# Kernel optimization log

Measured on AMD Instinct MI355X. Metric: run time of the kernel, lower is better.

The kernel has to match this reference:

```python
import jax, jax.numpy as jnp
import numpy as np
from jax import lax

DN = ('NCHW', 'OIHW', 'NCHW')
NUM_HEADS = 6


def _conv1x1(x, w):
    return lax.conv_general_dilated(x, w, (1, 1), 'VALID', dimension_numbers=DN)


def _dwconv3x3(x, w):
    # depthwise 3x3, groups == channels, padding 1
    return lax.conv_general_dilated(x, w, (1, 1), ((1, 1), (1, 1)),
                                    dimension_numbers=DN,
                                    feature_group_count=w.shape[0])


def setup_inputs() -> dict:
    key = jax.random.key(0)
    ks = jax.random.split(key, 7)
    b, dim, h, w = 4, 192, 128, 128
    inp = {
        'x': jax.random.normal(ks[0], (b, dim, h, w), jnp.float32),
        'ref': jax.random.normal(ks[1], (b, dim, h, w), jnp.float32),
        'w_qkv': jax.random.normal(ks[2], (dim * 3, dim, 1, 1), jnp.float32) * 0.05,
        'w_dw': jax.random.normal(ks[3], (dim * 3, 1, 3, 3), jnp.float32) * 0.1,
        'w_proj': jax.random.normal(ks[4], (dim, dim, 1, 1), jnp.float32) * 0.05,
        'temperature': jnp.ones((NUM_HEADS, 1, 1), jnp.float32),
        'attn_w': 0.2 * jnp.ones((4,), jnp.float32),
    }
    return inp


def reference(x, ref, w_qkv, w_dw, w_proj, temperature, attn_w):
    b, c, h, w = x.shape
    heads = NUM_HEADS
    C = c // heads  # per-head channel dim
    hw = h * w

    qkv = _dwconv3x3(_conv1x1(x, w_qkv), w_dw)        # [b, 3c, h, w]
    ref_qkv = _dwconv3x3(_conv1x1(ref, w_qkv), w_dw)  # shared weights

    q_shared = qkv[:, :c]            # q from x
    k_shared = ref_qkv[:, c:2 * c]   # k from ref
    v_shared = ref_qkv[:, 2 * c:]    # v from ref

    def to_heads(t):  # [b, c, h, w] -> [b, head, C, hw]
        return t.reshape(b, heads, C, hw)

    q = to_heads(q_shared)
    k = to_heads(k_shared)
    v = to_heads(v_shared)

    # L2-normalize along token dim (last axis)
    q = q / jnp.maximum(jnp.linalg.norm(q, axis=-1, keepdims=True), 1e-12)
    k = k / jnp.maximum(jnp.linalg.norm(k, axis=-1, keepdims=True), 1e-12)

    # channel-wise attention: [b, head, C, C]
    attn = jnp.einsum('bhcn,bhdn->bhcd', q, k) * temperature

    ks_list = [int(C / 2), int(C * 2 / 3), int(C * 3 / 4), int(C * 4 / 5)]
    neg_inf = jnp.asarray(-jnp.inf, attn.dtype)

    out = 0.0
    for i, ki in enumerate(ks_list):
        vals = lax.top_k(attn, ki)[0]            # [b, head, C, ki]
        thr = vals[..., -1:]                     # k-th largest per row
        a = jnp.where(attn >= thr, attn, neg_inf)
        a = jax.nn.softmax(a, axis=-1)
        out = out + attn_w[i] * jnp.einsum('bhcd,bhdn->bhcn', a, v)

    out = out.reshape(b, c, h, w)
    return _conv1x1(out, w_proj)
```

## Files before the change

### kernel.cpp

```cpp
#include <hip/hip_runtime.h>
#include <cstdint>
#include <cstddef>

typedef unsigned short u16;
typedef unsigned int u32;
typedef __attribute__((ext_vector_type(2))) float f32x2;
typedef __attribute__((ext_vector_type(4))) float f32x4;
typedef __attribute__((ext_vector_type(8))) short short8;
typedef __attribute__((ext_vector_type(2))) u32 u32x2;
typedef __attribute__((ext_vector_type(4))) u32 u32x4;

#define DEV static __device__ __forceinline__
#define HW 16384

DEV u16 f2bf(float f) {
  u32 u = __float_as_uint(f);
  u = (u + 0x7fffu + ((u >> 16) & 1u)) >> 16;
  return (u16)u;
}
DEV float bf2f(u16 h) { return __uint_as_float(((u32)h) << 16); }

DEV u32 packsplit(float f) {
  u16 h = f2bf(f);
  u16 l = f2bf(f - bf2f(h));
  return (u32)h | ((u32)l << 16);
}
DEV void unpack8(const u32* w, short8& hi, short8& lo) {
  #pragma unroll
  for (int i = 0; i < 8; ++i) {
    hi[i] = (short)(u16)w[i];
    lo[i] = (short)(u16)(w[i] >> 16);
  }
}
DEV void mfma3(f32x4& acc, short8 ah, short8 al, short8 bh, short8 bl) {
  acc = __builtin_amdgcn_mfma_f32_16x16x32_bf16(ah, bh, acc, 0, 0, 0);
  acc = __builtin_amdgcn_mfma_f32_16x16x32_bf16(ah, bl, acc, 0, 0, 0);
  acc = __builtin_amdgcn_mfma_f32_16x16x32_bf16(al, bh, acc, 0, 0, 0);
}

__global__ __launch_bounds__(256) void ksplit(const float* __restrict__ in,
                                              u32* __restrict__ out, int n) {
  int i = blockIdx.x * 256 + threadIdx.x;
  if (i < n) out[i] = packsplit(in[i]);
}

template<int ABATCH, int BPACKED, int MFRAG>
__global__ __launch_bounds__(512, 4) void gemm2(const u32* __restrict__ Asp,
                                                const u32* __restrict__ B,
                                                float* __restrict__ C) {
  constexpr int BM = MFRAG * 32;
  __shared__ u32 As[BM * 34];
  __shared__ u32 Bs[64 * 34];
  const int t = threadIdx.x, lane = t & 63, wid = t >> 6;
  const int b = blockIdx.z, n0 = blockIdx.x * 64;
  const u32* Ab = ABATCH ? (Asp + (size_t)b * 192 * 192) : Asp;
  const u32* Bb = B + (size_t)b * 192 * (size_t)HW;
  float* Cb = C + (size_t)b * BM * (size_t)HW;
  const int wr = wid >> 2, wc = wid & 3;
  const int g = lane >> 4, r16 = lane & 15;
  const int b_n = (t & 15) * 4, b_k = t >> 4;
  f32x4 acc[MFRAG] = {};

  u32x4 Breg, Bnext;
  u32x4 Areg[MFRAG / 2];
  Breg = *(const u32x4*)&Bb[(size_t)b_k * HW + n0 + b_n];
  #pragma unroll
  for (int i = 0; i < MFRAG / 2; ++i) {
    int vi = t + i * 512;
    Areg[i] = *(const u32x4*)&Ab[(size_t)(vi >> 3) * 192 + ((vi & 7) << 2)];
  }
  #pragma unroll 1
  for (int p = 0; p < 6; ++p) {
    #pragma unroll
    for (int j = 0; j < 4; ++j)
      Bs[(b_n + j) * 34 + b_k] = BPACKED ? Breg[j] : packsplit(__uint_as_float(Breg[j]));
    #pragma unroll
    for (int i = 0; i < MFRAG / 2; ++i) {
      int vi = t + i * 512;
      int row = vi >> 3, kc = (vi & 7) << 2;
      u32x2 v0 = {Areg[i][0], Areg[i][1]};
      u32x2 v1 = {Areg[i][2], Areg[i][3]};
      *(u32x2*)&As[row * 34 + kc] = v0;
      *(u32x2*)&As[row * 34 + kc + 2] = v1;
    }
    if (p < 5)
      Bnext = *(const u32x4*)&Bb[(size_t)((p + 1) * 32 + b_k) * HW + n0 + b_n];
    __syncthreads();
    if (p < 5) {
      #pragma unroll
      for (int i = 0; i < MFRAG / 2; ++i) {
        int vi = t + i * 512;
        Areg[i] = *(const u32x4*)&Ab[(size_t)(vi >> 3) * 192 + (p + 1) * 32 + ((vi & 7) << 2)];
      }
    }
    u32 bw[8];
    {
      const u32* bp = &Bs[(wc * 16 + r16) * 34 + g * 8];
      *(u32x2*)&bw[0] = *(const u32x2*)&bp[0];
      *(u32x2*)&bw[2] = *(const u32x2*)&bp[2];
      *(u32x2*)&bw[4] = *(const u32x2*)&bp[4];
      *(u32x2*)&bw[6] = *(const u32x2*)&bp[6];
    }
    short8 bh, bl; unpack8(bw, bh, bl);
    #pragma unroll
    for (int mf = 0; mf < MFRAG; ++mf) {
      u32 aw[8];
      const u32* ap = &As[(wr * (MFRAG * 16) + mf * 16 + r16) * 34 + g * 8];
      *(u32x2*)&aw[0] = *(const u32x2*)&ap[0];
      *(u32x2*)&aw[2] = *(const u32x2*)&ap[2];
      *(u32x2*)&aw[4] = *(const u32x2*)&ap[4];
      *(u32x2*)&aw[6] = *(const u32x2*)&ap[6];
      short8 ah, al; unpack8(aw, ah, al);
      acc[mf] = __builtin_amdgcn_mfma_f32_16x16x32_bf16(ah, bh, acc[mf], 0, 0, 0);
      acc[mf] = __builtin_amdgcn_mfma_f32_16x16x32_bf16(ah, bl, acc[mf], 0, 0, 0);
      acc[mf] = __builtin_amdgcn_mfma_f32_16x16x32_bf16(al, bh, acc[mf], 0, 0, 0);
    }
    __syncthreads();
    Breg = Bnext;
  }
  #pragma unroll
  for (int mf = 0; mf < MFRAG; ++mf)
    #pragma unroll
    for (int rr = 0; rr < 4; ++rr)
      Cb[(size_t)(wr * (MFRAG * 16) + mf * 16 + g * 4 + rr) * HW + n0 + wc * 16 + r16] =
          acc[mf][rr];
}

template<int SSQ>
__global__ __launch_bounds__(512) void k2_dw(const float* __restrict__ Tin, int cstIn,
                                             const float* __restrict__ wdw, int wco,
                                             u32* __restrict__ O,
                                             float* __restrict__ ssq, int sspath) {
  const int rt = blockIdx.x, cg = blockIdx.y, b = blockIdx.z;
  const int t = threadIdx.x, lane = t & 63, w = t >> 6;
  __shared__ float In[8][10][132];
  for (int idx = t; idx < 10400; idx += 512) {
    int ch = idx / 1300, rem = idx % 1300;
    int r = rem / 130, ci = rem % 130;
    int gr = rt * 8 + r - 1, gc = ci - 1;
    float v = 0.f;
    if (gr >= 0 && gr < 128 && gc >= 0 && gc < 128)
      v = Tin[((size_t)b * cstIn + cg * 8 + ch) * HW + gr * 128 + gc];
    In[ch][r][ci] = v;
  }
  float wv[9];
  #pragma unroll
  for (int j = 0; j < 9; ++j) wv[j] = wdw[(size_t)(wco + cg * 8 + w) * 9 + j];
  __syncthreads();
  float s = 0.f;
  u32* Op = O + ((size_t)b * 192 + cg * 8 + w) * HW + rt * 8 * 128 + 2 * lane;
  #pragma unroll
  for (int i = 0; i < 8; ++i) {
    float a0 = 0.f, a1 = 0.f;
    #pragma unroll
    for (int dr = 0; dr < 3; ++dr) {
      f32x2 u0 = *(const f32x2*)&In[w][i + dr][2 * lane];
      f32x2 u1 = *(const f32x2*)&In[w][i + dr][2 * lane + 2];
      a0 += wv[dr * 3] * u0[0] + wv[dr * 3 + 1] * u0[1] + wv[dr * 3 + 2] * u1[0];
      a1 += wv[dr * 3] * u0[1] + wv[dr * 3 + 1] * u1[0] + wv[dr * 3 + 2] * u1[1];
    }
    u32x2 o = {packsplit(a0), packsplit(a1)};
    *(u32x2*)&Op[(size_t)i * 128] = o;
    if (SSQ) s += a0 * a0 + a1 * a1;
  }
  if (SSQ) {
    #pragma unroll
    for (int off = 32; off; off >>= 1) s += __shfl_down(s, off);
    if (lane == 0) ssq[(((size_t)b * 2 + sspath) * 192 + cg * 8 + w) * 16 + rt] = s;
  }
}

__global__ __launch_bounds__(256) void k3_gram(const u32* __restrict__ q,
                                               const u32* __restrict__ k,
                                               float* __restrict__ gp) {
  const int ck = blockIdx.x, bh = blockIdx.y;
  const int b = bh / 6, h = bh % 6;
  const int t = threadIdx.x, lane = t & 63, wid = t >> 6;
  const int r16 = lane & 15, g = lane >> 4;
  const int chunk = ck * 4 + wid;
  const size_t rbase = ((size_t)b * 192 + h * 32 + r16) * HW;
  const u32* qp = q + rbase;
  const u32* kp = k + rbase;
  __shared__ float red[4][1024];
  f32x4 acc[2][2] = {};
  #pragma unroll 1
  for (int s = 0; s < 8; ++s) {
    int n = chunk * 256 + s * 32 + g * 8;
    u32 wq0[8], wq1[8], wk0[8], wk1[8];
    *(u32x4*)&wq0[0] = *(const u32x4*)&qp[n];
    *(u32x4*)&wq0[4] = *(const u32x4*)&qp[n + 4];
    *(u32x4*)&wq1[0] = *(const u32x4*)&qp[(size_t)16 * HW + n];
    *(u32x4*)&wq1[4] = *(const u32x4*)&qp[(size_t)16 * HW + n + 4];
    *(u32x4*)&wk0[0] = *(const u32x4*)&kp[n];
    *(u32x4*)&wk0[4] = *(const u32x4*)&kp[n + 4];
    *(u32x4*)&wk1[0] = *(const u32x4*)&kp[(size_t)16 * HW + n];
    *(u32x4*)&wk1[4] = *(const u32x4*)&kp[(size_t)16 * HW + n + 4];
    short8 a0h, a0l, a1h, a1l, b0h, b0l, b1h, b1l;
    unpack8(wq0, a0h, a0l);
    unpack8(wq1, a1h, a1l);
    unpack8(wk0, b0h, b0l);
    unpack8(wk1, b1h, b1l);
    mfma3(acc[0][0], a0h, a0l, b0h, b0l);
    mfma3(acc[0][1], a0h, a0l, b1h, b1l);
    mfma3(acc[1][0], a1h, a1l, b0h, b0l);
    mfma3(acc[1][1], a1h, a1l, b1h, b1l);
  }
  #pragma unroll
  for (int mf = 0; mf < 2; ++mf)
    #pragma unroll
    for (int nf = 0; nf < 2; ++nf)
      #pragma unroll
      for (int rr = 0; rr < 4; ++rr)
        red[wid][(mf * 16 + g * 4 + rr) * 32 + nf * 16 + r16] = acc[mf][nf][rr];
  __syncthreads();
  float* outp = gp + ((size_t)bh * 16 + ck) * 1024;
  #pragma unroll
  for (int e = t; e < 1024; e += 256)
    outp[e] = red[0][e] + red[1][e] + red[2][e] + red[3][e];
}

__global__ __launch_bounds__(512) void k4_comb(const float* __restrict__ gp,
                                               const float* __restrict__ ssq,
                                               const float* __restrict__ temp,
                                               const float* __restrict__ aw,
                                               const float* __restrict__ wproj,
                                               u32* __restrict__ mcp) {
  const int bh = blockIdx.x, b = bh / 6, h = bh % 6;
  const int t = threadIdx.x;
  __shared__ float Gs[1024];
  __shared__ float Acm[1024];
  __shared__ float Wp[192 * 32];
  __shared__ float nq[32], nk[32];
  #pragma unroll
  for (int i = 0; i < 3; ++i) {
    int idx = t + i * 512;
    int row = idx >> 3, c4 = (idx & 7) << 2;
    *(f32x4*)&Wp[row * 32 + c4] = *(const f32x4*)&wproj[(size_t)row * 192 + h * 32 + c4];
  }
  {
    const float* p = gp + (size_t)bh * 16 * 1024 + 2 * t;
    f32x2 s = {};
    #pragma unroll
    for (int ch = 0; ch < 16; ++ch) {
      f32x2 v = *(const f32x2*)&p[(size_t)ch * 1024];
      s[0] += v[0]; s[1] += v[1];
    }
    *(f32x2*)&Gs[2 * t] = s;
  }
  if (t < 64) {
    int c = t & 31, pk = t >> 5;
    const float* sp = ssq + (((size_t)b * 2 + pk) * 192 + h * 32 + c) * 16;
    f32x4 s4 = {};
    #pragma unroll
    for (int i = 0; i < 4; ++i) {
      f32x4 v = *(const f32x4*)&sp[4 * i];
      s4[0] += v[0]; s4[1] += v[1]; s4[2] += v[2]; s4[3] += v[3];
    }
    float nr = fmaxf(sqrtf(s4[0] + s4[1] + s4[2] + s4[3]), 1e-12f);
    if (pk == 0) nq[c] = nr; else nk[c] = nr;
  }
  __syncthreads();
  const float T = temp[h];
  {
    int c = (2 * t) >> 5;
    f32x2 v = *(const f32x2*)&Gs[2 * t];
    float inq = T / nq[c];
    v[0] = v[0] * inq / nk[(2 * t) & 31];
    v[1] = v[1] * inq / nk[(2 * t + 1) & 31];
    __syncthreads();
    *(f32x2*)&Gs[2 * t] = v;
  }
  __syncthreads();
  const float aw0 = aw[0], aw1 = aw[1], aw2 = aw[2], aw3 = aw[3];
  const int half = t >> 5, d = t & 31;
  #pragma unroll
  for (int it = 0; it < 2; ++it) {
    const int c = it * 16 + half;
    const float v = Gs[c * 32 + d];
    int cnt = 0;
    #pragma unroll
    for (int dd = 0; dd < 32; ++dd) cnt += (Gs[c * 32 + dd] >= v) ? 1 : 0;
    float c0 = v;
    float c1 = (cnt >= 16) ? v : -3.0e38f;
    float c2 = (cnt >= 21) ? v : -3.0e38f;
    float c3 = (cnt >= 24) ? v : -3.0e38f;
    float c4 = (cnt >= 25) ? v : -3.0e38f;
    #pragma unroll
    for (int off = 16; off; off >>= 1) {
      c0 = fmaxf(c0, __shfl_xor(c0, off));
      c1 = fmaxf(c1, __shfl_xor(c1, off));
      c2 = fmaxf(c2, __shfl_xor(c2, off));
      c3 = fmaxf(c3, __shfl_xor(c3, off));
      c4 = fmaxf(c4, __shfl_xor(c4, off));
    }
    const float m = c0;
    const float ex = expf(v - m);
    float z1 = (v >= c1) ? ex : 0.f;
    float z2 = (v >= c2) ? ex : 0.f;
    float z3 = (v >= c3) ? ex : 0.f;
    float z4 = (v >= c4) ? ex : 0.f;
    #pragma unroll
    for (int off = 16; off; off >>= 1) {
      z1 += __shfl_xor(z1, off);
      z2 += __shfl_xor(z2, off);
      z3 += __shfl_xor(z3, off);
      z4 += __shfl_xor(z4, off);
    }
    float a = 0.f;
    a += (v >= c1) ? aw0 * ex / z1 : 0.f;
    a += (v >= c2) ? aw1 * ex / z2 : 0.f;
    a += (v >= c3) ? aw2 * ex / z3 : 0.f;
    a += (v >= c4) ? aw3 * ex / z4 : 0.f;
    Acm[c * 32 + d] = a;
  }
  __syncthreads();
  #pragma unroll
  for (int i = 0; i < 12; ++i) {
    int idx = t + i * 512;
    int co = idx >> 5, dd = idx & 31;
    float s = 0.f;
    #pragma unroll
    for (int c = 0; c < 32; ++c) s += Wp[co * 32 + c] * Acm[c * 32 + dd];
    mcp[((size_t)b * 192 + co) * 192 + h * 32 + dd] = packsplit(s);
  }
}

extern "C" void kernel_launch(void* const* d_in, const int* in_sizes, int n_in,
                              void* d_out, int out_size, void* d_ws, size_t ws_size,
                              hipStream_t stream) {
  const float* x     = (const float*)d_in[0];
  const float* ref   = (const float*)d_in[1];
  const float* wqkv  = (const float*)d_in[2];
  const float* wdw   = (const float*)d_in[3];
  const float* wproj = (const float*)d_in[4];
  const float* temp  = (const float*)d_in[5];
  const float* aw    = (const float*)d_in[6];
  float* out = (float*)d_out;
  char* ws = (char*)d_ws;

  const size_t S = (size_t)4 * 192 * HW * 4;
  float* tA  = (float*)(ws);
  float* tKV = (float*)(ws + S);
  u32*   qpk = (u32*)(ws + 3 * S);
  float* gp  = (float*)(ws + 4 * S);
  float* ssq = (float*)(ws + 4 * S + 1572864);
  u32*   wsp = (u32*)(ws + 4 * S + 1572864 + 98304);
  u32*   mcp = (u32*)(ws + 4 * S + 1572864 + 98304 + 442368);
  u32*   kpk = (u32*)tA;
  u32*   vpk = qpk;

  ksplit<<<dim3(432), 256, 0, stream>>>(wqkv, wsp, 576 * 192);
  gemm2<0, 0, 6><<<dim3(256, 1, 4), 512, 0, stream>>>(wsp, (const u32*)x, tA);
  k2_dw<1><<<dim3(16, 24, 4), 512, 0, stream>>>(tA, 192, wdw, 0, qpk, ssq, 0);
  gemm2<0, 0, 12><<<dim3(256, 1, 4), 512, 0, stream>>>(wsp + 192 * 192, (const u32*)ref, tKV);
  k2_dw<1><<<dim3(16, 24, 4), 512, 0, stream>>>(tKV, 384, wdw, 192, kpk, ssq, 1);
  k3_gram<<<dim3(16, 24), 256, 0, stream>>>(qpk, kpk, gp);
  k2_dw<0><<<dim3(16, 24, 4), 512, 0, stream>>>(tKV + (size_t)192 * HW, 384, wdw, 384, vpk, nullptr, 2);
  k4_comb<<<dim3(24), 512, 0, stream>>>(gp, ssq, temp, aw, wproj, mcp);
  gemm2<1, 1, 6><<<dim3(256, 1, 4), 512, 0, stream>>>(mcp, vpk, out);
}
```

Before: 233.0 us.

## Store bf16 hi/lo planes separately in LDS and split 384-row GEMM across blocks

The GEMM kernel now keeps the hi and lo bf16 halves of each split operand in separate shared-memory arrays with a padded stride of 40. The MFMA fragments are then read as single 16-byte short8 loads, with no per-fragment unpack step. The 384-output-channel K/V projection is now split across two blocks along M (192 rows each) instead of one block holding 12 fragments. This lowers register pressure and adds parallelism, but the B tile is re-read from global memory by both M blocks.

```diff
diff --git a/kernel.cpp b/kernel.cpp
--- a/kernel.cpp
+++ b/kernel.cpp
@@ -44,73 +44,70 @@
   if (i < n) out[i] = packsplit(in[i]);
 }
 
-template<int ABATCH, int BPACKED, int MFRAG>
-__global__ __launch_bounds__(512, 4) void gemm2(const u32* __restrict__ Asp,
+template<int ABATCH, int BPACKED, int MT>
+__global__ __launch_bounds__(512, 4) void gemm3(const u32* __restrict__ Asp,
                                                 const u32* __restrict__ B,
                                                 float* __restrict__ C) {
-  constexpr int BM = MFRAG * 32;
-  __shared__ u32 As[BM * 34];
-  __shared__ u32 Bs[64 * 34];
+  __shared__ u16 Ah[192 * 40];
+  __shared__ u16 Al[192 * 40];
+  __shared__ u16 Bh[64 * 40];
+  __shared__ u16 Bl[64 * 40];
   const int t = threadIdx.x, lane = t & 63, wid = t >> 6;
-  const int b = blockIdx.z, n0 = blockIdx.x * 64;
-  const u32* Ab = ABATCH ? (Asp + (size_t)b * 192 * 192) : Asp;
+  const int b = blockIdx.z, n0 = blockIdx.x * 64, m0 = blockIdx.y * 192;
+  const u32* Ab = Asp + (ABATCH ? (size_t)b * 192 * 192 : 0) + (size_t)m0 * 192;
   const u32* Bb = B + (size_t)b * 192 * (size_t)HW;
-  float* Cb = C + (size_t)b * BM * (size_t)HW;
+  float* Cb = C + ((size_t)b * MT + m0) * (size_t)HW;
   const int wr = wid >> 2, wc = wid & 3;
   const int g = lane >> 4, r16 = lane & 15;
   const int b_n = (t & 15) * 4, b_k = t >> 4;
-  f32x4 acc[MFRAG] = {};
+  f32x4 acc[6] = {};
 
   u32x4 Breg, Bnext;
-  u32x4 Areg[MFRAG / 2];
+  u32x4 Areg[3];
   Breg = *(const u32x4*)&Bb[(size_t)b_k * HW + n0 + b_n];
   #pragma unroll
-  for (int i = 0; i < MFRAG / 2; ++i) {
+  for (int i = 0; i < 3; ++i) {
     int vi = t + i * 512;
     Areg[i] = *(const u32x4*)&Ab[(size_t)(vi >> 3) * 192 + ((vi & 7) << 2)];
   }
   #pragma unroll 1
   for (int p = 0; p < 6; ++p) {
     #pragma unroll
-    for (int j = 0; j < 4; ++j)
-      Bs[(b_n + j) * 34 + b_k] = BPACKED ? Breg[j] : packsplit(__uint_as_float(Breg[j]));
-    #pragma unroll
-    for (int i = 0; i < MFRAG / 2; ++i) {
+    for (int j = 0; j < 4; ++j) {
+      u32 w = BPACKED ? Breg[j] : packsplit(__uint_as_float(Breg[j]));
+      Bh[(b_n + j) * 40 + b_k] = (u16)w;
+      Bl[(b_n + j) * 40 + b_k] = (u16)(w >> 16);
+    }
+    #pragma unroll
+    for (int i = 0; i < 3; ++i) {
       int vi = t + i * 512;
       int row = vi >> 3, kc = (vi & 7) << 2;
-      u32x2 v0 = {Areg[i][0], Areg[i][1]};
-      u32x2 v1 = {Areg[i][2], Areg[i][3]};
-      *(u32x2*)&As[row * 34 + kc] = v0;
-      *(u32x2*)&As[row * 34 + kc + 2] = v1;
+      u32 h01 = (Areg[i][0] & 0xffffu) | (Areg[i][1] << 16);
+      u32 h23 = (Areg[i][2] & 0xffffu) | (Areg[i][3] << 16);
+      u32 l01 = (Areg[i][0] >> 16) | (Areg[i][1] & 0xffff0000u);
+      u32 l23 = (Areg[i][2] >> 16) | (Areg[i][3] & 0xffff0000u);
+      u32x2 hq = {h01, h23}, lq = {l01, l23};
+      *(u32x2*)&Ah[row * 40 + kc] = hq;
+      *(u32x2*)&Al[row * 40 + kc] = lq;
     }
     if (p < 5)
       Bnext = *(const u32x4*)&Bb[(size_t)((p + 1) * 32 + b_k) * HW + n0 + b_n];
     __syncthreads();
     if (p < 5) {
       #pragma unroll
-      for (int i = 0; i < MFRAG / 2; ++i) {
+      for (int i = 0; i < 3; ++i) {
         int vi = t + i * 512;
         Areg[i] = *(const u32x4*)&Ab[(size_t)(vi >> 3) * 192 + (p + 1) * 32 + ((vi & 7) << 2)];
       }
     }
-    u32 bw[8];
-    {
-      const u32* bp = &Bs[(wc * 16 + r16) * 34 + g * 8];
-      *(u32x2*)&bw[0] = *(const u32x2*)&bp[0];
-      *(u32x2*)&bw[2] = *(const u32x2*)&bp[2];
-      *(u32x2*)&bw[4] = *(const u32x2*)&bp[4];
-      *(u32x2*)&bw[6] = *(const u32x2*)&bp[6];
-    }
-    short8 bh, bl; unpack8(bw, bh, bl);
-    #pragma unroll
-    for (int mf = 0; mf < MFRAG; ++mf) {
-      u32 aw[8];
-      const u32* ap = &As[(wr * (MFRAG * 16) + mf * 16 + r16) * 34 + g * 8];
-      *(u32x2*)&aw[0] = *(const u32x2*)&ap[0];
-      *(u32x2*)&aw[2] = *(const u32x2*)&ap[2];
-      *(u32x2*)&aw[4] = *(const u32x2*)&ap[4];
-      *(u32x2*)&aw[6] = *(const u32x2*)&ap[6];
-      short8 ah, al; unpack8(aw, ah, al);
+    const int brow = (wc * 16 + r16) * 40 + g * 8;
+    short8 bh = *(const short8*)&Bh[brow];
+    short8 bl = *(const short8*)&Bl[brow];
+    #pragma unroll
+    for (int mf = 0; mf < 6; ++mf) {
+      const int arow = (wr * 96 + mf * 16 + r16) * 40 + g * 8;
+      short8 ah = *(const short8*)&Ah[arow];
+      short8 al = *(const short8*)&Al[arow];
       acc[mf] = __builtin_amdgcn_mfma_f32_16x16x32_bf16(ah, bh, acc[mf], 0, 0, 0);
       acc[mf] = __builtin_amdgcn_mfma_f32_16x16x32_bf16(ah, bl, acc[mf], 0, 0, 0);
       acc[mf] = __builtin_amdgcn_mfma_f32_16x16x32_bf16(al, bh, acc[mf], 0, 0, 0);
@@ -119,10 +116,10 @@
     Breg = Bnext;
   }
   #pragma unroll
-  for (int mf = 0; mf < MFRAG; ++mf)
+  for (int mf = 0; mf < 6; ++mf)
     #pragma unroll
     for (int rr = 0; rr < 4; ++rr)
-      Cb[(size_t)(wr * (MFRAG * 16) + mf * 16 + g * 4 + rr) * HW + n0 + wc * 16 + r16] =
+      Cb[(size_t)(wr * 96 + mf * 16 + g * 4 + rr) * HW + n0 + wc * 16 + r16] =
           acc[mf][rr];
 }
 
@@ -350,12 +347,12 @@
   u32*   vpk = qpk;
 
   ksplit<<<dim3(432), 256, 0, stream>>>(wqkv, wsp, 576 * 192);
-  gemm2<0, 0, 6><<<dim3(256, 1, 4), 512, 0, stream>>>(wsp, (const u32*)x, tA);
+  gemm3<0, 0, 192><<<dim3(256, 1, 4), 512, 0, stream>>>(wsp, (const u32*)x, tA);
   k2_dw<1><<<dim3(16, 24, 4), 512, 0, stream>>>(tA, 192, wdw, 0, qpk, ssq, 0);
-  gemm2<0, 0, 12><<<dim3(256, 1, 4), 512, 0, stream>>>(wsp + 192 * 192, (const u32*)ref, tKV);
+  gemm3<0, 0, 384><<<dim3(256, 2, 4), 512, 0, stream>>>(wsp + 192 * 192, (const u32*)ref, tKV);
   k2_dw<1><<<dim3(16, 24, 4), 512, 0, stream>>>(tKV, 384, wdw, 192, kpk, ssq, 1);
   k3_gram<<<dim3(16, 24), 256, 0, stream>>>(qpk, kpk, gp);
   k2_dw<0><<<dim3(16, 24, 4), 512, 0, stream>>>(tKV + (size_t)192 * HW, 384, wdw, 384, vpk, nullptr, 2);
   k4_comb<<<dim3(24), 512, 0, stream>>>(gp, ssq, temp, aw, wproj, mcp);
-  gemm2<1, 1, 6><<<dim3(256, 1, 4), 512, 0, stream>>>(mcp, vpk, out);
-}
+  gemm3<1, 1, 192><<<dim3(256, 1, 4), 512, 0, stream>>>(mcp, vpk, out);
+}
```

Result: slower. 252.1 us (+8.2%).
